# Optimization experiments

Hardware: AMD Instinct MI355X
Metric: run time of the kernel (lower is better)

## Reference

```python
import jax, jax.numpy as jnp
import numpy as np

TEMPERATURE = 0.1
B, D, A = 8192, 256, 4


def setup_inputs() -> dict:
    key = jax.random.key(0)
    k1, k2 = jax.random.split(key)
    # scale by 1/sqrt(D) so dot products are O(1) and exp(sim/T) is finite
    embeddings = jax.random.normal(k1, (B, D), dtype=jnp.float32) / jnp.sqrt(jnp.float32(D))
    labels = jax.random.randint(k2, (B, A), 0, 6, dtype=jnp.int64)
    return {"embeddings": embeddings, "labels": labels}


def reference(embeddings, labels):
    b = embeddings.shape[0]
    # [B, B] similarity scaled by temperature
    sim = jnp.matmul(embeddings, embeddings.T) / TEMPERATURE
    # positive mask: ANY aspect matches (vectorized over aspects), diagonal zeroed
    pos_mask = jnp.any(labels[:, None, :] == labels[None, :, :], axis=-1)
    pos_mask = pos_mask & ~jnp.eye(b, dtype=bool)
    pos_mask = pos_mask.astype(sim.dtype)

    exp_sim = jnp.exp(sim)
    positive_sim = jnp.sum(exp_sim * pos_mask, axis=1)            # [B]
    all_sim = jnp.sum(exp_sim, axis=1) - jnp.diagonal(exp_sim)   # [B]

    valid = positive_sim > 0
    pos_safe = jnp.where(valid, positive_sim, 1.0)
    all_safe = jnp.where(valid, all_sim, 1.0)
    row_loss = jnp.where(valid, -jnp.log(pos_safe / (all_safe + 1e-8)), 0.0)

    num_pos = jnp.sum(valid.astype(sim.dtype))
    loss = jnp.where(num_pos > 0, jnp.sum(row_loss) / jnp.maximum(num_pos, 1.0), 0.0)
    return loss
```

## Files before the change

### kernel.cpp

```cpp
#include <hip/hip_runtime.h>
#include <stdint.h>

typedef short short8 __attribute__((ext_vector_type(8)));
typedef float f32x4 __attribute__((ext_vector_type(4)));

#define B_TOTAL 8192
#define DDIM 256
#define BM 128
#define BN 64
#define NSPLIT 8
#define COLS_PER (B_TOTAL / NSPLIT)
#define ITERS (COLS_PER / BN)
#define EXP2_SCALE 14.426950408889634f

typedef __attribute__((address_space(3))) char lds_char;
typedef __attribute__((address_space(1))) const char gbl_char;

__device__ __forceinline__ unsigned short f2bf(float f) {
  unsigned int u = __builtin_bit_cast(unsigned int, f);
  u = (u + 0x7FFFu + ((u >> 16) & 1u)) >> 16;
  return (unsigned short)u;
}

__global__ __launch_bounds__(256) void prep_all(
    const float* __restrict__ E, const int* __restrict__ lab,
    unsigned short* __restrict__ Eb, unsigned int* __restrict__ plab,
    float* __restrict__ posAll) {
  const int t = blockIdx.x * 256 + threadIdx.x;
  const float4* s4 = (const float4*)E + (size_t)t * 2;
  float4 v0 = s4[0], v1 = s4[1];
  short8 o;
  o[0] = (short)f2bf(v0.x); o[1] = (short)f2bf(v0.y);
  o[2] = (short)f2bf(v0.z); o[3] = (short)f2bf(v0.w);
  o[4] = (short)f2bf(v1.x); o[5] = (short)f2bf(v1.y);
  o[6] = (short)f2bf(v1.z); o[7] = (short)f2bf(v1.w);
  *(short8*)(Eb + (size_t)t * 8) = o;
  if (t < B_TOTAL) {
    int4 l = ((const int4*)lab)[t];
    plab[t] = (unsigned int)(l.x & 0xFF) | ((unsigned int)(l.y & 0xFF) << 8)
            | ((unsigned int)(l.z & 0xFF) << 16) | ((unsigned int)(l.w & 0xFF) << 24);
  }
  if (t < 2 * B_TOTAL) posAll[t] = 0.0f;
}

struct __align__(16) SMem {
  char btile[BN * DDIM * 2];
  unsigned int plds[BN];
};

template <int DIAG>
__device__ __forceinline__ void do_epilogue(
    const f32x4 (&acc)[4][2], int colbase, int l15,
    const unsigned int (&pi)[2][4], const int (&irow)[2][4],
    const unsigned int* plds, float (&pos_s)[2][4], float (&all_s)[2][4]) {
#pragma unroll
  for (int n = 0; n < 4; ++n) {
    const int j = colbase + n * 16 + l15;
    const unsigned int pj = plds[n * 16 + l15];
#pragma unroll
    for (int m = 0; m < 2; ++m) {
#pragma unroll
      for (int q = 0; q < 4; ++q) {
        float e = exp2f(acc[n][m][q] * EXP2_SCALE);
        if (DIAG) { if (j == irow[m][q]) e = 0.0f; }
        unsigned int x = pi[m][q] ^ pj;
        unsigned int tz = (x - 0x01010101u) & ~x & 0x80808080u;
        all_s[m][q] += e;
        pos_s[m][q] += tz ? e : 0.0f;
      }
    }
  }
}

__global__ __launch_bounds__(256, 2) void main_kernel(
    const unsigned short* __restrict__ Eb, const unsigned int* __restrict__ plab,
    float* __restrict__ posArr, float* __restrict__ allArr) {
  __shared__ SMem sm;
  const int tid = threadIdx.x;
  const int lane = tid & 63;
  const int wid = tid >> 6;
  const int l15 = lane & 15;
  const int l4 = lane >> 4;
  const int rb = (int)blockIdx.x & 63;
  const int cs = (int)blockIdx.x >> 6;
  const int rowbase = rb * BM;
  const int colstart = cs * COLS_PER;

  short8 afrag[2][8];
#pragma unroll
  for (int m = 0; m < 2; ++m) {
    const int row = rowbase + wid * 32 + m * 16 + l15;
    const unsigned short* rp = Eb + (size_t)row * DDIM + l4 * 8;
#pragma unroll
    for (int k = 0; k < 8; ++k) afrag[m][k] = *(const short8*)(rp + k * 32);
  }

  unsigned int pi[2][4];
  int irow[2][4];
#pragma unroll
  for (int m = 0; m < 2; ++m)
#pragma unroll
    for (int q = 0; q < 4; ++q) {
      const int i = rowbase + wid * 32 + m * 16 + l4 * 4 + q;
      irow[m][q] = i;
      pi[m][q] = plab[i];
    }

  float pos_s[2][4] = {};
  float all_s[2][4] = {};

  for (int it = 0; it < ITERS; ++it) {
    const int colbase = colstart + it * BN;
    __syncthreads();
#pragma unroll
    for (int q = 0; q < 8; ++q) {
      const unsigned int L = (unsigned int)wid * 8192u + (unsigned int)q * 1024u +
                             (unsigned int)lane * 16u;
      const unsigned int r = L >> 9;
      const unsigned int s = (L >> 4) & 31u;
      const unsigned int c = s ^ (r & 7u);
      const char* src = (const char*)(Eb + (size_t)(colbase + (int)r) * DDIM + c * 8);
      char* dst = sm.btile + (unsigned int)wid * 8192u + (unsigned int)q * 1024u;
      __builtin_amdgcn_global_load_lds((gbl_char*)src, (lds_char*)dst, 16, 0, 0);
    }
    if (tid < BN) sm.plds[tid] = plab[colbase + tid];
    __syncthreads();

    f32x4 acc[4][2];
#pragma unroll
    for (int n = 0; n < 4; ++n)
#pragma unroll
      for (int m = 0; m < 2; ++m) acc[n][m] = (f32x4){0.f, 0.f, 0.f, 0.f};

#pragma unroll
    for (int k = 0; k < 8; ++k) {
      short8 b[4];
#pragma unroll
      for (int n = 0; n < 4; ++n) {
        const unsigned int rr = (unsigned int)(n * 16 + l15);
        const unsigned int cdx = (unsigned int)(k * 4 + l4);
        const unsigned int s = cdx ^ (rr & 7u);
        b[n] = *(const short8*)(sm.btile + rr * 512u + s * 16u);
      }
#pragma unroll
      for (int n = 0; n < 4; ++n)
#pragma unroll
        for (int m = 0; m < 2; ++m)
          acc[n][m] = __builtin_amdgcn_mfma_f32_16x16x32_bf16(
              afrag[m][k], b[n], acc[n][m], 0, 0, 0);
    }

    const bool hasDiag = (colbase < rowbase + BM) && (rowbase < colbase + BN);
    if (hasDiag)
      do_epilogue<1>(acc, colbase, l15, pi, irow, sm.plds, pos_s, all_s);
    else
      do_epilogue<0>(acc, colbase, l15, pi, irow, sm.plds, pos_s, all_s);
  }

#pragma unroll
  for (int m = 0; m < 2; ++m)
#pragma unroll
    for (int q = 0; q < 4; ++q) {
      float p = pos_s[m][q], al = all_s[m][q];
      p += __shfl_xor(p, 1); p += __shfl_xor(p, 2);
      p += __shfl_xor(p, 4); p += __shfl_xor(p, 8);
      al += __shfl_xor(al, 1); al += __shfl_xor(al, 2);
      al += __shfl_xor(al, 4); al += __shfl_xor(al, 8);
      if (l15 == 0) {
        atomicAdd(&posArr[irow[m][q]], p);
        atomicAdd(&allArr[irow[m][q]], al);
      }
    }
}

__global__ __launch_bounds__(1024) void finalize_kernel(
    const float* __restrict__ posArr, const float* __restrict__ allArr,
    float* __restrict__ out) {
  float ls = 0.f, cnt = 0.f;
#pragma unroll
  for (int k = 0; k < 8; ++k) {
    const int i = threadIdx.x + k * 1024;
    const float p = posArr[i];
    const float al = allArr[i];
    if (p > 0.f) { ls += -logf(p / (al + 1e-8f)); cnt += 1.f; }
  }
  for (int m = 1; m < 64; m <<= 1) { ls += __shfl_xor(ls, m); cnt += __shfl_xor(cnt, m); }
  __shared__ float sls[16], scnt[16];
  const int w = threadIdx.x >> 6;
  if ((threadIdx.x & 63) == 0) { sls[w] = ls; scnt[w] = cnt; }
  __syncthreads();
  if (threadIdx.x == 0) {
    float L = 0.f, C = 0.f;
    for (int i = 0; i < 16; ++i) { L += sls[i]; C += scnt[i]; }
    out[0] = (C > 0.f) ? L / fmaxf(C, 1.f) : 0.f;
  }
}

extern "C" void kernel_launch(void* const* d_in, const int* in_sizes, int n_in,
                              void* d_out, int out_size, void* d_ws, size_t ws_size,
                              hipStream_t stream) {
  const float* E = (const float*)d_in[0];
  const int* lab = (const int*)d_in[1];
  float* out = (float*)d_out;
  char* ws = (char*)d_ws;

  unsigned short* Eb = (unsigned short*)ws;
  unsigned int* plab = (unsigned int*)(ws + 4u * 1024u * 1024u);
  float* posArr = (float*)(ws + 4u * 1024u * 1024u + 32u * 1024u);
  float* allArr = posArr + B_TOTAL;

  prep_all<<<1024, 256, 0, stream>>>(E, lab, Eb, plab, posArr);
  main_kernel<<<(B_TOTAL / BM) * NSPLIT, 256, 0, stream>>>(Eb, plab, posArr, allArr);
  finalize_kernel<<<1, 1024, 0, stream>>>(posArr, allArr, out);
}
```

Measured before the change: 120.3 us.

## Fold exp scale into bf16 prep, one-hot label masks, fuse finalize via last-block

Measured after the change: 265.0 us. 120% more time.

```diff
diff --git a/kernel.cpp b/kernel.cpp
--- a/kernel.cpp
+++ b/kernel.cpp
@@ -3,15 +3,18 @@
 
 typedef short short8 __attribute__((ext_vector_type(8)));
 typedef float f32x4 __attribute__((ext_vector_type(4)));
+typedef float f32x2 __attribute__((ext_vector_type(2)));
 
 #define B_TOTAL 8192
 #define DDIM 256
 #define BM 128
 #define BN 64
-#define NSPLIT 8
+#define NSPLIT 16
 #define COLS_PER (B_TOTAL / NSPLIT)
 #define ITERS (COLS_PER / BN)
-#define EXP2_SCALE 14.426950408889634f
+#define NBLOCKS ((B_TOTAL / BM) * NSPLIT)
+#define SCALE_HALF 3.79828546f
+#define LN2F 0.6931471805599453f
 
 typedef __attribute__((address_space(3))) char lds_char;
 typedef __attribute__((address_space(1))) const char gbl_char;
@@ -25,56 +28,66 @@
 __global__ __launch_bounds__(256) void prep_all(
     const float* __restrict__ E, const int* __restrict__ lab,
     unsigned short* __restrict__ Eb, unsigned int* __restrict__ plab,
-    float* __restrict__ posAll) {
+    float* __restrict__ posAll, unsigned int* __restrict__ ctr) {
   const int t = blockIdx.x * 256 + threadIdx.x;
   const float4* s4 = (const float4*)E + (size_t)t * 2;
   float4 v0 = s4[0], v1 = s4[1];
   short8 o;
-  o[0] = (short)f2bf(v0.x); o[1] = (short)f2bf(v0.y);
-  o[2] = (short)f2bf(v0.z); o[3] = (short)f2bf(v0.w);
-  o[4] = (short)f2bf(v1.x); o[5] = (short)f2bf(v1.y);
-  o[6] = (short)f2bf(v1.z); o[7] = (short)f2bf(v1.w);
+  o[0] = (short)f2bf(v0.x * SCALE_HALF); o[1] = (short)f2bf(v0.y * SCALE_HALF);
+  o[2] = (short)f2bf(v0.z * SCALE_HALF); o[3] = (short)f2bf(v0.w * SCALE_HALF);
+  o[4] = (short)f2bf(v1.x * SCALE_HALF); o[5] = (short)f2bf(v1.y * SCALE_HALF);
+  o[6] = (short)f2bf(v1.z * SCALE_HALF); o[7] = (short)f2bf(v1.w * SCALE_HALF);
   *(short8*)(Eb + (size_t)t * 8) = o;
   if (t < B_TOTAL) {
     int4 l = ((const int4*)lab)[t];
-    plab[t] = (unsigned int)(l.x & 0xFF) | ((unsigned int)(l.y & 0xFF) << 8)
-            | ((unsigned int)(l.z & 0xFF) << 16) | ((unsigned int)(l.w & 0xFF) << 24);
+    plab[t] = (1u << ((unsigned)l.x & 31u))
+            | (1u << (((unsigned)l.y & 31u) + 6u))
+            | (1u << (((unsigned)l.z & 31u) + 12u))
+            | (1u << (((unsigned)l.w & 31u) + 18u));
   }
   if (t < 2 * B_TOTAL) posAll[t] = 0.0f;
+  if (t == 0) ctr[0] = 0u;
 }
 
 struct __align__(16) SMem {
   char btile[BN * DDIM * 2];
   unsigned int plds[BN];
+  float red[8];
+  int lastFlag;
 };
 
 template <int DIAG>
 __device__ __forceinline__ void do_epilogue(
     const f32x4 (&acc)[4][2], int colbase, int l15,
     const unsigned int (&pi)[2][4], const int (&irow)[2][4],
-    const unsigned int* plds, float (&pos_s)[2][4], float (&all_s)[2][4]) {
+    const unsigned int* plds, f32x2 (&pos2)[2][2], f32x2 (&all2)[2][2]) {
 #pragma unroll
   for (int n = 0; n < 4; ++n) {
     const int j = colbase + n * 16 + l15;
-    const unsigned int pj = plds[n * 16 + l15];
+    const unsigned int hj = plds[n * 16 + l15];
 #pragma unroll
     for (int m = 0; m < 2; ++m) {
+      float e[4];
 #pragma unroll
       for (int q = 0; q < 4; ++q) {
-        float e = exp2f(acc[n][m][q] * EXP2_SCALE);
-        if (DIAG) { if (j == irow[m][q]) e = 0.0f; }
-        unsigned int x = pi[m][q] ^ pj;
-        unsigned int tz = (x - 0x01010101u) & ~x & 0x80808080u;
-        all_s[m][q] += e;
-        pos_s[m][q] += tz ? e : 0.0f;
+        float v = __builtin_amdgcn_exp2f(acc[n][m][q]);
+        if (DIAG) { if (j == irow[m][q]) v = 0.0f; }
+        e[q] = v;
       }
-    }
-  }
-}
-
-__global__ __launch_bounds__(256, 2) void main_kernel(
+      f32x2 p01 = { (pi[m][0] & hj) ? e[0] : 0.0f, (pi[m][1] & hj) ? e[1] : 0.0f };
+      f32x2 p23 = { (pi[m][2] & hj) ? e[2] : 0.0f, (pi[m][3] & hj) ? e[3] : 0.0f };
+      all2[m][0] += (f32x2){e[0], e[1]};
+      all2[m][1] += (f32x2){e[2], e[3]};
+      pos2[m][0] += p01;
+      pos2[m][1] += p23;
+    }
+  }
+}
+
+__global__ __launch_bounds__(256, 4) void main_kernel(
     const unsigned short* __restrict__ Eb, const unsigned int* __restrict__ plab,
-    float* __restrict__ posArr, float* __restrict__ allArr) {
+    float* __restrict__ posArr, float* __restrict__ allArr,
+    unsigned int* __restrict__ ctr, float* __restrict__ out) {
   __shared__ SMem sm;
   const int tid = threadIdx.x;
   const int lane = tid & 63;
@@ -106,8 +119,8 @@
       pi[m][q] = plab[i];
     }
 
-  float pos_s[2][4] = {};
-  float all_s[2][4] = {};
+  f32x2 pos2[2][2] = {};
+  f32x2 all2[2][2] = {};
 
   for (int it = 0; it < ITERS; ++it) {
     const int colbase = colstart + it * BN;
@@ -152,16 +165,16 @@
 
     const bool hasDiag = (colbase < rowbase + BM) && (rowbase < colbase + BN);
     if (hasDiag)
-      do_epilogue<1>(acc, colbase, l15, pi, irow, sm.plds, pos_s, all_s);
+      do_epilogue<1>(acc, colbase, l15, pi, irow, sm.plds, pos2, all2);
     else
-      do_epilogue<0>(acc, colbase, l15, pi, irow, sm.plds, pos_s, all_s);
+      do_epilogue<0>(acc, colbase, l15, pi, irow, sm.plds, pos2, all2);
   }
 
 #pragma unroll
   for (int m = 0; m < 2; ++m)
 #pragma unroll
     for (int q = 0; q < 4; ++q) {
-      float p = pos_s[m][q], al = all_s[m][q];
+      float p = pos2[m][q >> 1][q & 1], al = all2[m][q >> 1][q & 1];
       p += __shfl_xor(p, 1); p += __shfl_xor(p, 2);
       p += __shfl_xor(p, 4); p += __shfl_xor(p, 8);
       al += __shfl_xor(al, 1); al += __shfl_xor(al, 2);
@@ -171,27 +184,39 @@
         atomicAdd(&allArr[irow[m][q]], al);
       }
     }
-}
-
-__global__ __launch_bounds__(1024) void finalize_kernel(
-    const float* __restrict__ posArr, const float* __restrict__ allArr,
-    float* __restrict__ out) {
+
+  __threadfence();
+  if (tid == 0) {
+    unsigned int t = __hip_atomic_fetch_add(ctr, 1u, __ATOMIC_ACQ_REL,
+                                            __HIP_MEMORY_SCOPE_AGENT);
+    sm.lastFlag = (t == NBLOCKS - 1);
+  }
+  __syncthreads();
+  if (!sm.lastFlag) return;
+
   float ls = 0.f, cnt = 0.f;
 #pragma unroll
-  for (int k = 0; k < 8; ++k) {
-    const int i = threadIdx.x + k * 1024;
-    const float p = posArr[i];
-    const float al = allArr[i];
-    if (p > 0.f) { ls += -logf(p / (al + 1e-8f)); cnt += 1.f; }
-  }
-  for (int m = 1; m < 64; m <<= 1) { ls += __shfl_xor(ls, m); cnt += __shfl_xor(cnt, m); }
-  __shared__ float sls[16], scnt[16];
-  const int w = threadIdx.x >> 6;
-  if ((threadIdx.x & 63) == 0) { sls[w] = ls; scnt[w] = cnt; }
+  for (int k = 0; k < B_TOTAL / 256; ++k) {
+    const int i = tid + (k << 8);
+    const float p = __hip_atomic_load(&posArr[i], __ATOMIC_RELAXED,
+                                      __HIP_MEMORY_SCOPE_AGENT);
+    const float a = __hip_atomic_load(&allArr[i], __ATOMIC_RELAXED,
+                                      __HIP_MEMORY_SCOPE_AGENT);
+    if (p > 0.f) {
+      ls += (__builtin_amdgcn_logf(a + 1e-8f) - __builtin_amdgcn_logf(p)) * LN2F;
+      cnt += 1.f;
+    }
+  }
+#pragma unroll
+  for (int msk = 1; msk < 64; msk <<= 1) {
+    ls += __shfl_xor(ls, msk);
+    cnt += __shfl_xor(cnt, msk);
+  }
+  if (lane == 0) { sm.red[wid] = ls; sm.red[4 + wid] = cnt; }
   __syncthreads();
-  if (threadIdx.x == 0) {
-    float L = 0.f, C = 0.f;
-    for (int i = 0; i < 16; ++i) { L += sls[i]; C += scnt[i]; }
+  if (tid == 0) {
+    float L = sm.red[0] + sm.red[1] + sm.red[2] + sm.red[3];
+    float C = sm.red[4] + sm.red[5] + sm.red[6] + sm.red[7];
     out[0] = (C > 0.f) ? L / fmaxf(C, 1.f) : 0.f;
   }
 }
@@ -208,8 +233,8 @@
   unsigned int* plab = (unsigned int*)(ws + 4u * 1024u * 1024u);
   float* posArr = (float*)(ws + 4u * 1024u * 1024u + 32u * 1024u);
   float* allArr = posArr + B_TOTAL;
-
-  prep_all<<<1024, 256, 0, stream>>>(E, lab, Eb, plab, posArr);
-  main_kernel<<<(B_TOTAL / BM) * NSPLIT, 256, 0, stream>>>(Eb, plab, posArr, allArr);
-  finalize_kernel<<<1, 1024, 0, stream>>>(posArr, allArr, out);
-}
+  unsigned int* ctr = (unsigned int*)(allArr + B_TOTAL);
+
+  prep_all<<<1024, 256, 0, stream>>>(E, lab, Eb, plab, posArr, ctr);
+  main_kernel<<<NBLOCKS, 256, 0, stream>>>(Eb, plab, posArr, allArr, ctr, out);
+}
```
